# Kernel tuning notes

Measured on AMD Instinct MI355X. Metric: run time of the kernel, lower is better.

## Reference

```python
import jax, jax.numpy as jnp
import numpy as np

B, TQ, TK, D, H = 4, 2048, 2048, 512, 8
NEG = -1e9
LN_EPS = 1e-3  # Keras LayerNormalization default


def setup_inputs() -> dict:
    key = jax.random.key(0)
    ks = jax.random.split(key, 5)
    s = 0.02
    return {
        "queries": jax.random.normal(ks[0], (B, TQ, D), jnp.float32),
        "keys_in": jax.random.normal(ks[1], (B, TK, D), jnp.float32),
        "Wq": jax.random.normal(ks[2], (D, D), jnp.float32) * s,
        "bq": jnp.zeros((D,), jnp.float32),
        "Wk": jax.random.normal(ks[3], (D, D), jnp.float32) * s,
        "bk": jnp.zeros((D,), jnp.float32),
        "Wv": jax.random.normal(ks[4], (D, D), jnp.float32) * s,
        "bv": jnp.zeros((D,), jnp.float32),
        "gamma": jnp.ones((D,), jnp.float32),
        "beta": jnp.zeros((D,), jnp.float32),
    }


def reference(queries, keys_in, Wq, bq, Wk, bk, Wv, bv, gamma, beta):
    # Dense projections with relu activation (as in the original layer)
    Q = jax.nn.relu(queries @ Wq + bq)   # [B, Tq, D]
    K = jax.nn.relu(keys_in @ Wk + bk)   # [B, Tk, D]
    V = jax.nn.relu(keys_in @ Wv + bv)   # [B, Tk, D]

    b, tq, d = Q.shape
    tk = K.shape[1]
    dh = d // H
    # split_heads: tf.split(axis=-1)+concat(axis=0) == contiguous feature chunks per head
    Qh = Q.reshape(b, tq, H, dh)
    Kh = K.reshape(b, tk, H, dh)
    Vh = V.reshape(b, tk, H, dh)

    scores = jnp.einsum('bqhd,bkhd->bhqk', Qh, Kh) / jnp.sqrt(jnp.float32(dh))

    # key padding mask derived from per-head K content: sum(|K|) > 0 along dh
    kmask = jnp.sum(jnp.abs(Kh), axis=-1) > 0            # [B, Tk, H]
    kmask = jnp.transpose(kmask, (0, 2, 1))              # [B, H, Tk]
    scores = jnp.where(kmask[:, :, None, :], scores, NEG)

    attn = jax.nn.softmax(scores, axis=-1)               # [B, H, Tq, Tk]

    # query mask: zero out attention rows for all-zero query positions
    qmask = (jnp.sum(jnp.abs(Qh), axis=-1) > 0).astype(attn.dtype)  # [B, Tq, H]
    qmask = jnp.transpose(qmask, (0, 2, 1))              # [B, H, Tq]
    attn = attn * qmask[:, :, :, None]

    out = jnp.einsum('bhqk,bkhd->bqhd', attn, Vh).reshape(b, tq, d)

    # residual + LayerNorm (Keras default: last axis, eps=1e-3)
    res = out + queries
    mu = jnp.mean(res, axis=-1, keepdims=True)
    var = jnp.var(res, axis=-1, keepdims=True)
    return (res - mu) * jax.lax.rsqrt(var + LN_EPS) * gamma + beta
```

## Files before the change

### kernel.cpp

```cpp
#include <hip/hip_runtime.h>
#include <cstdint>

#define BB 4
#define TT 2048
#define DD 512
#define HH 8
#define DH 64
#define NT (TT / 64)
#define LOG2E 1.4426950408889634f

using bf16x8 = __attribute__((ext_vector_type(8))) __bf16;
using f32x4  = __attribute__((ext_vector_type(4))) float;
using us8    = __attribute__((ext_vector_type(8))) unsigned short;
using us4    = __attribute__((ext_vector_type(4))) unsigned short;
using u32x2  = __attribute__((ext_vector_type(2))) unsigned int;

typedef const __attribute__((address_space(1))) unsigned int* as1cp;
typedef __attribute__((address_space(3))) unsigned int* as3p;

__device__ __forceinline__ void gload16(const void* g, void* l) {
  __builtin_amdgcn_global_load_lds((as1cp)(uintptr_t)g,
                                   (as3p)(unsigned int)(uintptr_t)l, 16, 0, 0);
}

__device__ __forceinline__ unsigned short f2bf(float x) {
  unsigned int u = __float_as_uint(x);
  u += 0x7fffu + ((u >> 16) & 1u);
  return (unsigned short)(u >> 16);
}
__device__ __forceinline__ float bf2f(unsigned short u) {
  return __uint_as_float(((unsigned int)u) << 16);
}
__device__ __forceinline__ f32x4 MFMA(bf16x8 a, bf16x8 b, f32x4 c) {
  return __builtin_amdgcn_mfma_f32_16x16x32_bf16(a, b, c, 0, 0, 0);
}

#define WAITVM(N) asm volatile("s_waitcnt vmcnt(" #N ")" ::: "memory")
#define RAWBAR() asm volatile("s_barrier" ::: "memory")

__global__ __launch_bounds__(256) void prep_kernel(const float4* __restrict__ q,
                                                   const float4* __restrict__ k,
                                                   us4* __restrict__ qb,
                                                   us4* __restrict__ kb,
                                                   const float* __restrict__ Wq,
                                                   const float* __restrict__ Wk,
                                                   const float* __restrict__ Wv,
                                                   unsigned short* __restrict__ Wt) {
  __shared__ float tile[32][33];
  int id = blockIdx.x;
  if (id < 4096) {
    size_t i = (size_t)id * 256 + threadIdx.x;
    float4 a = q[i];
    us4 o; o[0] = f2bf(a.x); o[1] = f2bf(a.y); o[2] = f2bf(a.z); o[3] = f2bf(a.w);
    qb[i] = o;
    float4 b = k[i];
    us4 p; p[0] = f2bf(b.x); p[1] = f2bf(b.y); p[2] = f2bf(b.z); p[3] = f2bf(b.w);
    kb[i] = p;
  } else {
    int id2 = id - 4096;
    int z = id2 >> 8, rem = id2 & 255;
    const float* W = (z == 0) ? Wq : (z == 1) ? Wk : Wv;
    int k0 = (rem & 15) * 32, n0 = (rem >> 4) * 32;
    int r = threadIdx.x >> 5, c = threadIdx.x & 31;
#pragma unroll
    for (int p = 0; p < 4; ++p)
      tile[r + p * 8][c] = W[(size_t)(k0 + r + p * 8) * DD + n0 + c];
    __syncthreads();
    unsigned short* o = Wt + (size_t)z * DD * DD;
#pragma unroll
    for (int p = 0; p < 4; ++p)
      o[(size_t)(n0 + r + p * 8) * DD + k0 + c] = f2bf(tile[c][r + p * 8]);
  }
}

__global__ __launch_bounds__(256) void gemm_proj(const unsigned short* __restrict__ qb,
                                                 const unsigned short* __restrict__ kb,
                                                 const unsigned short* __restrict__ Wt,
                                                 const float* __restrict__ bq,
                                                 const float* __restrict__ bk,
                                                 const float* __restrict__ bv,
                                                 unsigned short* __restrict__ Qp,
                                                 unsigned short* __restrict__ Kp,
                                                 unsigned short* __restrict__ Vp) {
  int z = blockIdx.z;
  const unsigned short* A  = (z == 0) ? qb : kb;
  const unsigned short* Bt = Wt + (size_t)z * DD * DD;
  const float* bias = (z == 0) ? bq : (z == 1) ? bk : bv;
  unsigned short* out = (z == 0) ? Qp : (z == 1) ? Kp : Vp;
  const float osc = (z == 0) ? 0.125f * LOG2E : 1.0f;

  __shared__ __align__(16) unsigned short As[128 * 32];
  __shared__ __align__(16) unsigned short Bs[128 * 32];

  int mb = blockIdx.x * 128, nb = blockIdx.y * 128;
  int w = threadIdx.x >> 6, lane = threadIdx.x & 63;
  int l15 = lane & 15, lg = lane >> 4;
  int wr = (w >> 1) * 64, wc = (w & 1) * 64;

  f32x4 acc[4][4] = {};

  for (int kt = 0; kt < DD / 32; ++kt) {
    int kk = kt * 32;
    int t = threadIdx.x;
#pragma unroll
    for (int it = 0; it < 2; ++it) {
      int c = t + it * 256;
      gload16(A  + (size_t)(mb + (c >> 2)) * DD + kk + (c & 3) * 8, As + c * 8);
      gload16(Bt + (size_t)(nb + (c >> 2)) * DD + kk + (c & 3) * 8, Bs + c * 8);
    }
    __syncthreads();
    bf16x8 af[4], bf[4];
#pragma unroll
    for (int m = 0; m < 4; ++m)
      af[m] = *(const bf16x8*)&As[(wr + m * 16 + l15) * 32 + lg * 8];
#pragma unroll
    for (int n = 0; n < 4; ++n)
      bf[n] = *(const bf16x8*)&Bs[(wc + n * 16 + l15) * 32 + lg * 8];
#pragma unroll
    for (int m = 0; m < 4; ++m)
#pragma unroll
      for (int n = 0; n < 4; ++n)
        acc[m][n] = MFMA(af[m], bf[n], acc[m][n]);
    __syncthreads();
  }

#pragma unroll
  for (int m = 0; m < 4; ++m)
#pragma unroll
    for (int n = 0; n < 4; ++n)
#pragma unroll
      for (int i = 0; i < 4; ++i) {
        int row = mb + wr + m * 16 + lg * 4 + i;
        int col = nb + wc + n * 16 + l15;
        float v = acc[m][n][i] + bias[col];
        out[(size_t)row * DD + col] = f2bf(fmaxf(v, 0.f) * osc);
      }
}

__global__ __launch_bounds__(256) void post_proj(const unsigned short* __restrict__ Qp,
                                                 const unsigned short* __restrict__ Kp,
                                                 const unsigned short* __restrict__ Vp,
                                                 unsigned short* __restrict__ Vt,
                                                 float* __restrict__ qmask,
                                                 uint2* __restrict__ kbits) {
  __shared__ unsigned short tile[64][72];
  int id = blockIdx.x;
  if (id < 1024) {
    int b = id >> 8, k0 = (id & 31) * 64, d0 = ((id >> 5) & 7) * 64;
    int t = threadIdx.x;
    int r = t >> 3, c8 = (t & 7) * 8;
#pragma unroll
    for (int p = 0; p < 2; ++p) {
      int row = r + p * 32;
      us8 v = *(const us8*)&Vp[(size_t)(b * TT + k0 + row) * DD + d0 + c8];
#pragma unroll
      for (int j = 0; j < 8; ++j) tile[row][c8 + j] = v[j];
    }
    __syncthreads();
#pragma unroll
    for (int p = 0; p < 2; ++p) {
      int dr = r + p * 32;
      us8 o;
#pragma unroll
      for (int j = 0; j < 8; ++j) o[j] = tile[c8 + j][dr];
      *(us8*)&Vt[((size_t)b * DD + d0 + dr) * TT + k0 + c8] = o;
    }
  } else {
    int wid = (id - 1024) * 4 + (threadIdx.x >> 6);
    int lane = threadIdx.x & 63;
    int side = wid >> 10;
    int rem = wid & 1023;
    int bh = rem >> 5, tl = rem & 31;
    int b = bh >> 3, h = bh & 7;
    const unsigned short* src =
        (side ? Kp : Qp) + ((size_t)(b * TT + tl * 64 + lane)) * DD + h * DH;
    float s = 0.f;
#pragma unroll
    for (int j = 0; j < 64; j += 8) {
      us8 v = *(const us8*)(src + j);
#pragma unroll
      for (int e = 0; e < 8; ++e) s += bf2f(v[e]);
    }
    if (side == 0) {
      qmask[(size_t)bh * TT + tl * 64 + lane] = (s > 0.f) ? 1.f : 0.f;
    } else {
      unsigned long long mb = __ballot(s > 0.f);
      if (lane == 0)
        kbits[bh * NT + tl] = make_uint2((unsigned int)mb, (unsigned int)(mb >> 32));
    }
  }
}

#define STAGE(tt, pbuf)                                                      \
  {                                                                          \
    int c0_ = threadIdx.x;                                                   \
    _Pragma("unroll")                                                        \
    for (int it_ = 0; it_ < 2; ++it_) {                                      \
      int c_ = c0_ + it_ * 256;                                              \
      int r_ = c_ >> 3, j_ = c_ & 7;                                         \
      int js_ = j_ ^ (r_ & 7);                                               \
      gload16(kg + (size_t)((tt) * 64 + r_) * DD + js_ * 8,                  \
              &KsBuf[pbuf][(size_t)c_ * 8]);                                 \
      gload16(vg + (size_t)r_ * TT + (tt) * 64 + js_ * 8,                    \
              &VsBuf[pbuf][(size_t)c_ * 8]);                                 \
    }                                                                        \
  }

__global__ __launch_bounds__(256) void attn_kernel(
    const unsigned short* __restrict__ Qp,
    const unsigned short* __restrict__ Kp,
    const unsigned short* __restrict__ Vt,
    const uint2* __restrict__ kbits,
    const float* __restrict__ qmask,
    float* __restrict__ O) {
  __shared__ __align__(16) unsigned short KsBuf[2][64 * 64];
  __shared__ __align__(16) unsigned short VsBuf[2][64 * 64];

  const int w = threadIdx.x >> 6;
  const int lane = threadIdx.x & 63;
  const int l15 = lane & 15, lg = lane >> 4;

  int flat = blockIdx.x;
  int wg = (flat & 7) * 128 + (flat >> 3);
  int qt = wg & 31, bh = wg >> 5;
  int h = bh & 7, b = bh >> 3;
  int q0 = qt * 64 + w * 16;

  const unsigned short* qbase =
      Qp + ((size_t)(b * TT + q0 + l15)) * DD + h * DH + lg * 8;
  bf16x8 qf0 = *(const bf16x8*)(qbase);
  bf16x8 qf1 = *(const bf16x8*)(qbase + 32);

  const unsigned short* kg = Kp + ((size_t)b * TT) * DD + h * DH;
  const unsigned short* vg = Vt + ((size_t)(b * DD + h * DH)) * TT;
  const uint2* kb_ptr = kbits + (size_t)bh * NT;

  const int krow_base = ((l15 & 12) << 1) | (l15 & 3);

  f32x4 oat[4] = {};
  float m_i = -1e30f, l_i = 0.f;

  STAGE(0, 0);

  for (int t = 0; t < NT; ++t) {
    int pb = t & 1;
    if (t + 1 < NT) {
      STAGE(t + 1, pb ^ 1);
      WAITVM(4);
    } else {
      WAITVM(0);
    }
    RAWBAR();

    const unsigned short* ksb = &KsBuf[pb][0];
    const unsigned short* vsb = &VsBuf[pb][0];

    f32x4 s[4];
    __builtin_amdgcn_s_setprio(1);
#pragma unroll
    for (int f = 0; f < 4; ++f) {
      int row = krow_base + ((f & 1) << 2) + ((f >> 1) << 5);
      int r7 = row & 7;
      bf16x8 k0 = *(const bf16x8*)&ksb[row * 64 + ((lg ^ r7) << 3)];
      bf16x8 k1 = *(const bf16x8*)&ksb[row * 64 + (((4 | lg) ^ r7) << 3)];
      f32x4 z = {};
      z = MFMA(k0, qf0, z);
      s[f] = MFMA(k1, qf1, z);
    }
    __builtin_amdgcn_s_setprio(0);

    bf16x8 vf[4][2];
#pragma unroll
    for (int fd = 0; fd < 4; ++fd) {
      int row = 16 * fd + l15;
      int r7 = l15 & 7;
      vf[fd][0] = *(const bf16x8*)&vsb[row * 64 + ((lg ^ r7) << 3)];
      vf[fd][1] = *(const bf16x8*)&vsb[row * 64 + (((4 | lg) ^ r7) << 3)];
    }

    uint2 kw = kb_ptr[t];
    if ((kw.x & kw.y) != 0xffffffffu) {
#pragma unroll
      for (int f = 0; f < 4; ++f) {
        unsigned int word = (f >> 1) ? kw.y : kw.x;
        unsigned int nib = (word >> (8 * lg + 4 * (f & 1))) & 0xFu;
#pragma unroll
        for (int i = 0; i < 4; ++i)
          if (!((nib >> i) & 1)) s[f][i] = -1e30f;
      }
    }

    float m0 = fmaxf(fmaxf(s[0][0], s[0][1]), fmaxf(s[0][2], s[0][3]));
    float m1 = fmaxf(fmaxf(s[1][0], s[1][1]), fmaxf(s[1][2], s[1][3]));
    float m2 = fmaxf(fmaxf(s[2][0], s[2][1]), fmaxf(s[2][2], s[2][3]));
    float m3 = fmaxf(fmaxf(s[3][0], s[3][1]), fmaxf(s[3][2], s[3][3]));
    float pm = fmaxf(fmaxf(m0, m1), fmaxf(m2, m3));
    pm = fmaxf(pm, __shfl_xor(pm, 16));
    u32x2 sw = __builtin_amdgcn_permlane32_swap(__float_as_uint(pm),
                                                __float_as_uint(pm), false, false);
    pm = fmaxf(__uint_as_float(sw[0]), __uint_as_float(sw[1]));

    if (__any(pm > m_i + 12.f)) {
      float mn = fmaxf(m_i, pm);
      float al = exp2f(m_i - mn);
      m_i = mn;
      l_i *= al;
#pragma unroll
      for (int f = 0; f < 4; ++f)
#pragma unroll
        for (int i = 0; i < 4; ++i) oat[f][i] *= al;
    }

    float a = 0.f;
#pragma unroll
    for (int f = 0; f < 4; ++f)
#pragma unroll
      for (int i = 0; i < 4; ++i) {
        float p = exp2f(fminf(s[f][i] - m_i, 30.f));
        s[f][i] = p;
        a += p;
      }
    a += __shfl_xor(a, 16);
    u32x2 sr = __builtin_amdgcn_permlane32_swap(__float_as_uint(a),
                                                __float_as_uint(a), false, false);
    a = __uint_as_float(sr[0]) + __uint_as_float(sr[1]);
    l_i += a;

    bf16x8 pb0v, pb1v;
#pragma unroll
    for (int f2 = 0; f2 < 2; ++f2)
#pragma unroll
      for (int i = 0; i < 4; ++i) {
        pb0v[f2 * 4 + i] = (__bf16)s[f2][i];
        pb1v[f2 * 4 + i] = (__bf16)s[2 + f2][i];
      }

    __builtin_amdgcn_s_setprio(1);
#pragma unroll
    for (int fd = 0; fd < 4; ++fd) {
      oat[fd] = MFMA(vf[fd][0], pb0v, oat[fd]);
      oat[fd] = MFMA(vf[fd][1], pb1v, oat[fd]);
    }
    __builtin_amdgcn_s_setprio(0);

    if (t + 1 < NT) RAWBAR();
  }

  float qm = qmask[(size_t)bh * TT + q0 + l15];
  float sc = qm / fmaxf(l_i, 1e-37f);
  float* ob = O + ((size_t)(b * TT + q0 + l15)) * DD + h * DH + 4 * lg;
#pragma unroll
  for (int fd = 0; fd < 4; ++fd) {
    float4 v = make_float4(oat[fd][0] * sc, oat[fd][1] * sc,
                           oat[fd][2] * sc, oat[fd][3] * sc);
    *(float4*)(ob + 16 * fd) = v;
  }
}

__global__ __launch_bounds__(256) void ln_kernel(const float* __restrict__ O,
                                                 const float* __restrict__ qin,
                                                 const float* __restrict__ gamma,
                                                 const float* __restrict__ beta,
                                                 float* __restrict__ out) {
  int row = blockIdx.x * 4 + (threadIdx.x >> 6);
  int lane = threadIdx.x & 63;
  size_t base = (size_t)row * DD + lane * 8;
  const float4* o4 = (const float4*)(O + base);
  const float4* q4 = (const float4*)(qin + base);
  float4 a = o4[0], b2 = o4[1], c = q4[0], d2 = q4[1];
  float v[8];
  v[0] = a.x + c.x; v[1] = a.y + c.y; v[2] = a.z + c.z; v[3] = a.w + c.w;
  v[4] = b2.x + d2.x; v[5] = b2.y + d2.y; v[6] = b2.z + d2.z; v[7] = b2.w + d2.w;
  float s = 0.f, s2 = 0.f;
#pragma unroll
  for (int j = 0; j < 8; ++j) { s += v[j]; s2 += v[j] * v[j]; }
#pragma unroll
  for (int xm = 1; xm < 64; xm <<= 1) {
    s += __shfl_xor(s, xm);
    s2 += __shfl_xor(s2, xm);
  }
  float mu = s * (1.0f / DD);
  float var = s2 * (1.0f / DD) - mu * mu;
  float rs = rsqrtf(var + 1e-3f);
  const float* g = gamma + lane * 8;
  const float* bb = beta + lane * 8;
  float* ob = out + base;
#pragma unroll
  for (int j = 0; j < 8; ++j) ob[j] = (v[j] - mu) * rs * g[j] + bb[j];
}

extern "C" void kernel_launch(void* const* d_in, const int* in_sizes, int n_in,
                              void* d_out, int out_size, void* d_ws, size_t ws_size,
                              hipStream_t stream) {
  (void)in_sizes; (void)n_in; (void)out_size; (void)ws_size;
  const float* queries = (const float*)d_in[0];
  const float* keys_in = (const float*)d_in[1];
  const float* Wq = (const float*)d_in[2];
  const float* bq = (const float*)d_in[3];
  const float* Wk = (const float*)d_in[4];
  const float* bk = (const float*)d_in[5];
  const float* Wv = (const float*)d_in[6];
  const float* bv = (const float*)d_in[7];
  const float* gamma = (const float*)d_in[8];
  const float* beta  = (const float*)d_in[9];
  float* out = (float*)d_out;

  char* ws = (char*)d_ws;
  unsigned short* qb = (unsigned short*)(ws);
  unsigned short* kb = (unsigned short*)(ws + (8ull << 20));
  float*          O  = (float*)(ws);
  unsigned short* Qp = (unsigned short*)(ws + (16ull << 20));
  unsigned short* Kp = (unsigned short*)(ws + (24ull << 20));
  unsigned short* Vp = (unsigned short*)(ws + (32ull << 20));
  unsigned short* Vt = (unsigned short*)(ws + (40ull << 20));
  unsigned short* Wt = (unsigned short*)(ws + (48ull << 20));
  float* qmaskp = (float*)(ws + (50ull << 20));
  uint2* kbitsp = (uint2*)(ws + (50ull << 20) + (512ull << 10));

  prep_kernel<<<4864, 256, 0, stream>>>((const float4*)queries, (const float4*)keys_in,
                                        (us4*)qb, (us4*)kb, Wq, Wk, Wv, Wt);
  gemm_proj<<<dim3(64, 4, 3), 256, 0, stream>>>(qb, kb, Wt, bq, bk, bv, Qp, Kp, Vp);
  post_proj<<<1536, 256, 0, stream>>>(Qp, Kp, Vp, Vt, qmaskp, kbitsp);
  attn_kernel<<<1024, 256, 0, stream>>>(Qp, Kp, Vt, kbitsp, qmaskp, O);
  ln_kernel<<<2048, 256, 0, stream>>>(O, queries, gamma, beta, out);
}
```

Before: 216.0 us.

## Switch attention to 32x32 MFMA tiles with split-K and merge in layernorm

The attention kernel now uses 32x32x16 MFMAs, with each wave handling 32 query rows instead of 16, so K/V tiles loaded from LDS are reused across more queries. The key dimension is split in two halves across workgroups, keeping the same grid size of 1024 while doubling the query tile. Each half writes a bf16 partial output plus its (m, l) softmax statistics. The layernorm kernel merges the two partials with rescaling and applies the query mask. This cuts LDS traffic per FLOP, but adds partial-output writes, the merge work, and some bf16 rounding of the intermediate output.

Measured after the change: 207.1 us. 1.04x faster.

```diff
diff --git a/kernel.cpp b/kernel.cpp
--- a/kernel.cpp
+++ b/kernel.cpp
@@ -11,6 +11,7 @@
 
 using bf16x8 = __attribute__((ext_vector_type(8))) __bf16;
 using f32x4  = __attribute__((ext_vector_type(4))) float;
+using f32x16 = __attribute__((ext_vector_type(16))) float;
 using us8    = __attribute__((ext_vector_type(8))) unsigned short;
 using us4    = __attribute__((ext_vector_type(4))) unsigned short;
 using u32x2  = __attribute__((ext_vector_type(2))) unsigned int;
@@ -33,6 +34,9 @@
 }
 __device__ __forceinline__ f32x4 MFMA(bf16x8 a, bf16x8 b, f32x4 c) {
   return __builtin_amdgcn_mfma_f32_16x16x32_bf16(a, b, c, 0, 0, 0);
+}
+__device__ __forceinline__ f32x16 MFMA32(bf16x8 a, bf16x8 b, f32x16 c) {
+  return __builtin_amdgcn_mfma_f32_32x32x16_bf16(a, b, c, 0, 0, 0);
 }
 
 #define WAITVM(N) asm volatile("s_waitcnt vmcnt(" #N ")" ::: "memory")
@@ -199,7 +203,8 @@
       int c_ = c0_ + it_ * 256;                                              \
       int r_ = c_ >> 3, j_ = c_ & 7;                                         \
       int js_ = j_ ^ (r_ & 7);                                               \
-      gload16(kg + (size_t)((tt) * 64 + r_) * DD + js_ * 8,                  \
+      int kr_ = (r_ & ~12) | ((r_ & 4) << 1) | ((r_ & 8) >> 1);              \
+      gload16(kg + (size_t)((tt) * 64 + kr_) * DD + js_ * 8,                 \
               &KsBuf[pbuf][(size_t)c_ * 8]);                                 \
       gload16(vg + (size_t)r_ * TT + (tt) * 64 + js_ * 8,                    \
               &VsBuf[pbuf][(size_t)c_ * 8]);                                 \
@@ -211,40 +216,40 @@
     const unsigned short* __restrict__ Kp,
     const unsigned short* __restrict__ Vt,
     const uint2* __restrict__ kbits,
-    const float* __restrict__ qmask,
-    float* __restrict__ O) {
+    unsigned short* __restrict__ Opart,
+    float2* __restrict__ ml) {
   __shared__ __align__(16) unsigned short KsBuf[2][64 * 64];
   __shared__ __align__(16) unsigned short VsBuf[2][64 * 64];
 
   const int w = threadIdx.x >> 6;
   const int lane = threadIdx.x & 63;
-  const int l15 = lane & 15, lg = lane >> 4;
+  const int l31 = lane & 31, h2 = lane >> 5;
 
   int flat = blockIdx.x;
   int wg = (flat & 7) * 128 + (flat >> 3);
-  int qt = wg & 31, bh = wg >> 5;
+  int s = wg & 1, qt = (wg >> 1) & 15, bh = wg >> 5;
   int h = bh & 7, b = bh >> 3;
-  int q0 = qt * 64 + w * 16;
+  int q0 = qt * 128 + w * 32;
 
   const unsigned short* qbase =
-      Qp + ((size_t)(b * TT + q0 + l15)) * DD + h * DH + lg * 8;
-  bf16x8 qf0 = *(const bf16x8*)(qbase);
-  bf16x8 qf1 = *(const bf16x8*)(qbase + 32);
+      Qp + ((size_t)(b * TT + q0 + l31)) * DD + h * DH + h2 * 8;
+  bf16x8 qf[4];
+#pragma unroll
+  for (int kd = 0; kd < 4; ++kd) qf[kd] = *(const bf16x8*)(qbase + kd * 16);
 
   const unsigned short* kg = Kp + ((size_t)b * TT) * DD + h * DH;
   const unsigned short* vg = Vt + ((size_t)(b * DD + h * DH)) * TT;
   const uint2* kb_ptr = kbits + (size_t)bh * NT;
 
-  const int krow_base = ((l15 & 12) << 1) | (l15 & 3);
-
-  f32x4 oat[4] = {};
+  f32x16 oat0 = {}, oat1 = {};
   float m_i = -1e30f, l_i = 0.f;
 
-  STAGE(0, 0);
-
-  for (int t = 0; t < NT; ++t) {
+  const int t0 = s * 16, t1 = t0 + 16;
+  STAGE(t0, 0);
+
+  for (int t = t0; t < t1; ++t) {
     int pb = t & 1;
-    if (t + 1 < NT) {
+    if (t + 1 < t1) {
       STAGE(t + 1, pb ^ 1);
       WAITVM(4);
     } else {
@@ -255,47 +260,41 @@
     const unsigned short* ksb = &KsBuf[pb][0];
     const unsigned short* vsb = &VsBuf[pb][0];
 
-    f32x4 s[4];
+    bf16x8 kf0[4], kf1[4];
+#pragma unroll
+    for (int kd = 0; kd < 4; ++kd) {
+      int j = kd * 2 + h2;
+      int x = (j ^ (l31 & 7)) << 3;
+      kf0[kd] = *(const bf16x8*)&ksb[l31 * 64 + x];
+      kf1[kd] = *(const bf16x8*)&ksb[(32 + l31) * 64 + x];
+    }
+    f32x16 s0 = {}, s1 = {};
     __builtin_amdgcn_s_setprio(1);
 #pragma unroll
-    for (int f = 0; f < 4; ++f) {
-      int row = krow_base + ((f & 1) << 2) + ((f >> 1) << 5);
-      int r7 = row & 7;
-      bf16x8 k0 = *(const bf16x8*)&ksb[row * 64 + ((lg ^ r7) << 3)];
-      bf16x8 k1 = *(const bf16x8*)&ksb[row * 64 + (((4 | lg) ^ r7) << 3)];
-      f32x4 z = {};
-      z = MFMA(k0, qf0, z);
-      s[f] = MFMA(k1, qf1, z);
-    }
+    for (int kd = 0; kd < 4; ++kd) s0 = MFMA32(kf0[kd], qf[kd], s0);
+#pragma unroll
+    for (int kd = 0; kd < 4; ++kd) s1 = MFMA32(kf1[kd], qf[kd], s1);
     __builtin_amdgcn_s_setprio(0);
-
-    bf16x8 vf[4][2];
-#pragma unroll
-    for (int fd = 0; fd < 4; ++fd) {
-      int row = 16 * fd + l15;
-      int r7 = l15 & 7;
-      vf[fd][0] = *(const bf16x8*)&vsb[row * 64 + ((lg ^ r7) << 3)];
-      vf[fd][1] = *(const bf16x8*)&vsb[row * 64 + (((4 | lg) ^ r7) << 3)];
-    }
 
     uint2 kw = kb_ptr[t];
     if ((kw.x & kw.y) != 0xffffffffu) {
 #pragma unroll
-      for (int f = 0; f < 4; ++f) {
-        unsigned int word = (f >> 1) ? kw.y : kw.x;
-        unsigned int nib = (word >> (8 * lg + 4 * (f & 1))) & 0xFu;
-#pragma unroll
-        for (int i = 0; i < 4; ++i)
-          if (!((nib >> i) & 1)) s[f][i] = -1e30f;
+      for (int r = 0; r < 16; ++r) {
+        int sh = ((r >> 3) << 4) + (h2 << 3) + (r & 7);
+        if (!((kw.x >> sh) & 1)) s0[r] = -1e30f;
+        if (!((kw.y >> sh) & 1)) s1[r] = -1e30f;
       }
     }
 
-    float m0 = fmaxf(fmaxf(s[0][0], s[0][1]), fmaxf(s[0][2], s[0][3]));
-    float m1 = fmaxf(fmaxf(s[1][0], s[1][1]), fmaxf(s[1][2], s[1][3]));
-    float m2 = fmaxf(fmaxf(s[2][0], s[2][1]), fmaxf(s[2][2], s[2][3]));
-    float m3 = fmaxf(fmaxf(s[3][0], s[3][1]), fmaxf(s[3][2], s[3][3]));
-    float pm = fmaxf(fmaxf(m0, m1), fmaxf(m2, m3));
-    pm = fmaxf(pm, __shfl_xor(pm, 16));
+    float x0 = fmaxf(fmaxf(fmaxf(s0[0], s0[1]), fmaxf(s0[2], s0[3])),
+                     fmaxf(fmaxf(s0[4], s0[5]), fmaxf(s0[6], s0[7])));
+    float x1 = fmaxf(fmaxf(fmaxf(s0[8], s0[9]), fmaxf(s0[10], s0[11])),
+                     fmaxf(fmaxf(s0[12], s0[13]), fmaxf(s0[14], s0[15])));
+    float x2 = fmaxf(fmaxf(fmaxf(s1[0], s1[1]), fmaxf(s1[2], s1[3])),
+                     fmaxf(fmaxf(s1[4], s1[5]), fmaxf(s1[6], s1[7])));
+    float x3 = fmaxf(fmaxf(fmaxf(s1[8], s1[9]), fmaxf(s1[10], s1[11])),
+                     fmaxf(fmaxf(s1[12], s1[13]), fmaxf(s1[14], s1[15])));
+    float pm = fmaxf(fmaxf(x0, x1), fmaxf(x2, x3));
     u32x2 sw = __builtin_amdgcn_permlane32_swap(__float_as_uint(pm),
                                                 __float_as_uint(pm), false, false);
     pm = fmaxf(__uint_as_float(sw[0]), __uint_as_float(sw[1]));
@@ -306,74 +305,103 @@
       m_i = mn;
       l_i *= al;
 #pragma unroll
-      for (int f = 0; f < 4; ++f)
-#pragma unroll
-        for (int i = 0; i < 4; ++i) oat[f][i] *= al;
-    }
-
-    float a = 0.f;
-#pragma unroll
-    for (int f = 0; f < 4; ++f)
-#pragma unroll
-      for (int i = 0; i < 4; ++i) {
-        float p = exp2f(fminf(s[f][i] - m_i, 30.f));
-        s[f][i] = p;
-        a += p;
-      }
-    a += __shfl_xor(a, 16);
-    u32x2 sr = __builtin_amdgcn_permlane32_swap(__float_as_uint(a),
-                                                __float_as_uint(a), false, false);
-    a = __uint_as_float(sr[0]) + __uint_as_float(sr[1]);
-    l_i += a;
-
-    bf16x8 pb0v, pb1v;
-#pragma unroll
-    for (int f2 = 0; f2 < 2; ++f2)
-#pragma unroll
-      for (int i = 0; i < 4; ++i) {
-        pb0v[f2 * 4 + i] = (__bf16)s[f2][i];
-        pb1v[f2 * 4 + i] = (__bf16)s[2 + f2][i];
-      }
+      for (int r = 0; r < 16; ++r) { oat0[r] *= al; oat1[r] *= al; }
+    }
+
+    float a0 = 0.f, a1 = 0.f, a2 = 0.f, a3 = 0.f;
+#pragma unroll
+    for (int r = 0; r < 8; ++r)  { float p = exp2f(fminf(s0[r] - m_i, 30.f)); s0[r] = p; a0 += p; }
+#pragma unroll
+    for (int r = 8; r < 16; ++r) { float p = exp2f(fminf(s0[r] - m_i, 30.f)); s0[r] = p; a1 += p; }
+#pragma unroll
+    for (int r = 0; r < 8; ++r)  { float p = exp2f(fminf(s1[r] - m_i, 30.f)); s1[r] = p; a2 += p; }
+#pragma unroll
+    for (int r = 8; r < 16; ++r) { float p = exp2f(fminf(s1[r] - m_i, 30.f)); s1[r] = p; a3 += p; }
+    float rs = (a0 + a1) + (a2 + a3);
+    u32x2 sr = __builtin_amdgcn_permlane32_swap(__float_as_uint(rs),
+                                                __float_as_uint(rs), false, false);
+    rs = __uint_as_float(sr[0]) + __uint_as_float(sr[1]);
+    l_i += rs;
+
+    bf16x8 vf0[4], vf1[4];
+#pragma unroll
+    for (int ks = 0; ks < 4; ++ks) {
+      int j = ks * 2 + h2;
+      int x = (j ^ (l31 & 7)) << 3;
+      vf0[ks] = *(const bf16x8*)&vsb[l31 * 64 + x];
+      vf1[ks] = *(const bf16x8*)&vsb[(32 + l31) * 64 + x];
+    }
+
+    bf16x8 pbf[4];
+#pragma unroll
+    for (int j = 0; j < 8; ++j) {
+      pbf[0][j] = (__bf16)s0[j];
+      pbf[1][j] = (__bf16)s0[8 + j];
+      pbf[2][j] = (__bf16)s1[j];
+      pbf[3][j] = (__bf16)s1[8 + j];
+    }
 
     __builtin_amdgcn_s_setprio(1);
 #pragma unroll
-    for (int fd = 0; fd < 4; ++fd) {
-      oat[fd] = MFMA(vf[fd][0], pb0v, oat[fd]);
-      oat[fd] = MFMA(vf[fd][1], pb1v, oat[fd]);
+    for (int ks = 0; ks < 4; ++ks) {
+      oat0 = MFMA32(vf0[ks], pbf[ks], oat0);
+      oat1 = MFMA32(vf1[ks], pbf[ks], oat1);
     }
     __builtin_amdgcn_s_setprio(0);
 
-    if (t + 1 < NT) RAWBAR();
-  }
-
-  float qm = qmask[(size_t)bh * TT + q0 + l15];
-  float sc = qm / fmaxf(l_i, 1e-37f);
-  float* ob = O + ((size_t)(b * TT + q0 + l15)) * DD + h * DH + 4 * lg;
-#pragma unroll
-  for (int fd = 0; fd < 4; ++fd) {
-    float4 v = make_float4(oat[fd][0] * sc, oat[fd][1] * sc,
-                           oat[fd][2] * sc, oat[fd][3] * sc);
-    *(float4*)(ob + 16 * fd) = v;
-  }
-}
-
-__global__ __launch_bounds__(256) void ln_kernel(const float* __restrict__ O,
-                                                 const float* __restrict__ qin,
-                                                 const float* __restrict__ gamma,
-                                                 const float* __restrict__ beta,
-                                                 float* __restrict__ out) {
+    if (t + 1 < t1) RAWBAR();
+  }
+
+  if (h2 == 0)
+    ml[((size_t)s * 32 + bh) * TT + q0 + l31] = make_float2(m_i, l_i);
+  unsigned short* op = Opart + (size_t)s * (32ull * TT * 64) +
+                       ((size_t)bh * TT + q0 + l31) * 64;
+#pragma unroll
+  for (int e = 0; e < 8; ++e) {
+    int r = e * 2;
+    int d = (r & 3) + 8 * (r >> 2) + 4 * h2;
+    unsigned int w0 = f2bf(oat0[r]) | ((unsigned int)f2bf(oat0[r + 1]) << 16);
+    *(unsigned int*)(op + d) = w0;
+    unsigned int w1 = f2bf(oat1[r]) | ((unsigned int)f2bf(oat1[r + 1]) << 16);
+    *(unsigned int*)(op + 32 + d) = w1;
+  }
+}
+
+__global__ __launch_bounds__(256) void ln_merge(const unsigned short* __restrict__ Opart,
+                                                const float2* __restrict__ ml,
+                                                const float* __restrict__ qmask,
+                                                const float* __restrict__ qin,
+                                                const float* __restrict__ gamma,
+                                                const float* __restrict__ beta,
+                                                float* __restrict__ out) {
   int row = blockIdx.x * 4 + (threadIdx.x >> 6);
-  int lane = threadIdx.x & 63;
-  size_t base = (size_t)row * DD + lane * 8;
-  const float4* o4 = (const float4*)(O + base);
+  int j = threadIdx.x & 63;
+  int b = row >> 11, q = row & (TT - 1);
+  int h = j >> 3, bh = b * 8 + h;
+  const size_t SSTR = 32ull * TT * 64;
+  size_t pidx = ((size_t)bh * TT + q) * 64 + (size_t)(j & 7) * 8;
+  us8 o0 = *(const us8*)(Opart + pidx);
+  us8 o1 = *(const us8*)(Opart + SSTR + pidx);
+  float2 ma = ml[(size_t)bh * TT + q];
+  float2 mb = ml[32ull * TT + (size_t)bh * TT + q];
+  float M = fmaxf(ma.x, mb.x);
+  float w0 = exp2f(ma.x - M), w1 = exp2f(mb.x - M);
+  float l = ma.y * w0 + mb.y * w1;
+  float qm = qmask[(size_t)bh * TT + q];
+  float sc = qm / fmaxf(l, 1e-30f);
+
+  size_t base = (size_t)row * DD + (size_t)j * 8;
   const float4* q4 = (const float4*)(qin + base);
-  float4 a = o4[0], b2 = o4[1], c = q4[0], d2 = q4[1];
+  float4 c = q4[0], d2 = q4[1];
+  float qv[8] = {c.x, c.y, c.z, c.w, d2.x, d2.y, d2.z, d2.w};
   float v[8];
-  v[0] = a.x + c.x; v[1] = a.y + c.y; v[2] = a.z + c.z; v[3] = a.w + c.w;
-  v[4] = b2.x + d2.x; v[5] = b2.y + d2.y; v[6] = b2.z + d2.z; v[7] = b2.w + d2.w;
+#pragma unroll
+  for (int e = 0; e < 8; ++e)
+    v[e] = (bf2f(o0[e]) * w0 + bf2f(o1[e]) * w1) * sc + qv[e];
+
   float s = 0.f, s2 = 0.f;
 #pragma unroll
-  for (int j = 0; j < 8; ++j) { s += v[j]; s2 += v[j] * v[j]; }
+  for (int e = 0; e < 8; ++e) { s += v[e]; s2 += v[e] * v[e]; }
 #pragma unroll
   for (int xm = 1; xm < 64; xm <<= 1) {
     s += __shfl_xor(s, xm);
@@ -381,12 +409,12 @@
   }
   float mu = s * (1.0f / DD);
   float var = s2 * (1.0f / DD) - mu * mu;
-  float rs = rsqrtf(var + 1e-3f);
-  const float* g = gamma + lane * 8;
-  const float* bb = beta + lane * 8;
+  float rsd = rsqrtf(var + 1e-3f);
+  const float* g = gamma + j * 8;
+  const float* bb = beta + j * 8;
   float* ob = out + base;
 #pragma unroll
-  for (int j = 0; j < 8; ++j) ob[j] = (v[j] - mu) * rs * g[j] + bb[j];
+  for (int e = 0; e < 8; ++e) ob[e] = (v[e] - mu) * rsd * g[e] + bb[e];
 }
 
 extern "C" void kernel_launch(void* const* d_in, const int* in_sizes, int n_in,
@@ -408,7 +436,7 @@
   char* ws = (char*)d_ws;
   unsigned short* qb = (unsigned short*)(ws);
   unsigned short* kb = (unsigned short*)(ws + (8ull << 20));
-  float*          O  = (float*)(ws);
+  unsigned short* Opart = (unsigned short*)(ws);
   unsigned short* Qp = (unsigned short*)(ws + (16ull << 20));
   unsigned short* Kp = (unsigned short*)(ws + (24ull << 20));
   unsigned short* Vp = (unsigned short*)(ws + (32ull << 20));
@@ -416,11 +444,12 @@
   unsigned short* Wt = (unsigned short*)(ws + (48ull << 20));
   float* qmaskp = (float*)(ws + (50ull << 20));
   uint2* kbitsp = (uint2*)(ws + (50ull << 20) + (512ull << 10));
+  float2* mlp   = (float2*)(ws + (51ull << 20));
 
   prep_kernel<<<4864, 256, 0, stream>>>((const float4*)queries, (const float4*)keys_in,
                                         (us4*)qb, (us4*)kb, Wq, Wk, Wv, Wt);
   gemm_proj<<<dim3(64, 4, 3), 256, 0, stream>>>(qb, kb, Wt, bq, bk, bv, Qp, Kp, Vp);
   post_proj<<<1536, 256, 0, stream>>>(Qp, Kp, Vp, Vt, qmaskp, kbitsp);
-  attn_kernel<<<1024, 256, 0, stream>>>(Qp, Kp, Vt, kbitsp, qmaskp, O);
-  ln_kernel<<<2048, 256, 0, stream>>>(O, queries, gamma, beta, out);
-}
+  attn_kernel<<<1024, 256, 0, stream>>>(Qp, Kp, Vt, kbitsp, Opart, mlp);
+  ln_merge<<<2048, 256, 0, stream>>>(Opart, mlp, qmaskp, queries, gamma, beta, out);
+}
```
